# Optimization experiments

Hardware: AMD Instinct MI355X
Metric: run time of the kernel (lower is better)

Reference implementation:

```python
import jax, jax.numpy as jnp
import numpy as np

B, N, H = 4, 4096, 64
T1 = 3072  # num_types = [0, 3072, 1024]


def _xavier(key, shape):
    fan_in, fan_out = shape[1], shape[0]
    lim = float(np.sqrt(6.0 / (fan_in + fan_out)))
    return jax.random.uniform(key, shape, jnp.float32, -lim, lim)


def setup_inputs() -> dict:
    key = jax.random.key(0)
    ks = jax.random.split(key, 16)
    adjacency = (jax.random.uniform(ks[0], (N, N)) < 0.05).astype(jnp.float32)
    adjacency = jnp.maximum(adjacency, jnp.eye(N, dtype=jnp.float32))  # avoid all-zero rows
    return {
        "hidden_states": jax.random.normal(ks[1], (B, N, H), jnp.float32),
        "input_states": jax.random.normal(ks[2], (B, 1, 1), jnp.float32),
        "adjacency": adjacency,
        "Wq": _xavier(ks[3], (H, H)),
        "Wk": _xavier(ks[4], (H, H)),
        "Wv": _xavier(ks[5], (H, H)),
        "Wu_inter": _xavier(ks[6], (H, H)),
        "bu_inter": jnp.zeros((H,), jnp.float32),
        "Wt_inter": _xavier(ks[7], (H, H)),
        "bt_inter": jnp.zeros((H,), jnp.float32),
        "Wu_out": _xavier(ks[8], (H, H)),
        "bu_out": jnp.zeros((H,), jnp.float32),
        "Wt_out": _xavier(ks[9], (H, H)),
        "bt_out": jnp.zeros((H,), jnp.float32),
        "step_size": jnp.float32(0.01),
    }


def reference(hidden_states, input_states, adjacency, Wq, Wk, Wv,
              Wu_inter, bu_inter, Wt_inter, bt_inter,
              Wu_out, bu_out, Wt_out, bt_out, step_size):
    # AccumulatorFunction: adjacency-masked QK^T, L2-norm rows (NOT softmax), aggregate V
    mask = adjacency.T  # [N, N]
    q = hidden_states @ Wq.T  # [B, N, H]
    k = hidden_states @ Wk.T
    v = hidden_states @ Wv.T
    rel = jnp.einsum('bnd,bmd->bnm', q, k) * mask  # [B, N, N]
    rel = rel / jnp.linalg.norm(rel, axis=2, keepdims=True)
    acc = jnp.einsum('bnm,bmd->bnd', rel, v)  # [B, N, H]

    # update_hidden_states with num_types = [0, T1, N - T1]
    def branch(h, a, Wu, bu, Wt, bt):
        dt = 2.0 * jax.nn.sigmoid(h @ Wt.T + bt) - 1.0
        return h + step_size * dt * (a @ Wu.T + bu)

    upd_inter = branch(hidden_states[:, :T1], acc[:, :T1],
                       Wu_inter, bu_inter, Wt_inter, bt_inter)
    upd_out = branch(hidden_states[:, T1:], acc[:, T1:],
                     Wu_out, bu_out, Wt_out, bt_out)
    return jnp.concatenate([upd_inter, upd_out], axis=1)  # [B, N, H]
```

## Files before the change

### kernel.cpp

```cpp
#include <hip/hip_runtime.h>
#include <hip/hip_bf16.h>
#include <math.h>

#define Bb 4
#define Nn 4096
#define Hh 64
#define T1c 3072
#define MC 8

typedef unsigned short ushort_t;
typedef __bf16 bf16x8 __attribute__((ext_vector_type(8)));
typedef float floatx4 __attribute__((ext_vector_type(4)));
typedef float floatx16 __attribute__((ext_vector_type(16)));

__device__ ushort_t g_qw[(size_t)Bb * Nn * Hh];
__device__ ushort_t g_kp[(size_t)Bb * Nn * Hh];
__device__ ushort_t g_vp[(size_t)Bb * Nn * Hh];
__device__ ushort_t g_dt[(size_t)Bb * Nn * Hh];
__device__ unsigned g_bm32[(size_t)(Nn / 32) * Nn];
__device__ ushort_t g_pacH[(size_t)Bb * 64 * MC * 64 * 64];
__device__ float    g_pss[(size_t)Bb * 64 * MC * 64];

__device__ __forceinline__ float bf2f(unsigned short u) {
    union { unsigned int i; float f; } c;
    c.i = ((unsigned int)u) << 16;
    return c.f;
}
__device__ __forceinline__ unsigned short f2bf(float f) {
    union { float f; unsigned int i; } c;
    c.f = f;
    unsigned int x = c.i;
    unsigned int r = (x + 0x7fffu + ((x >> 16) & 1u)) >> 16;
    return (unsigned short)r;
}

__device__ __forceinline__ bf16x8 ld8(const void* p, size_t eidx, bool f32) {
    if (f32) {
        const float* fp = (const float*)p + eidx;
        float4 x0 = *(const float4*)fp;
        float4 x1 = *(const float4*)(fp + 4);
        bf16x8 r;
        r[0] = (__bf16)x0.x; r[1] = (__bf16)x0.y; r[2] = (__bf16)x0.z; r[3] = (__bf16)x0.w;
        r[4] = (__bf16)x1.x; r[5] = (__bf16)x1.y; r[6] = (__bf16)x1.z; r[7] = (__bf16)x1.w;
        return r;
    }
    return *(const bf16x8*)((const ushort_t*)p + eidx);
}
__device__ __forceinline__ float ldS(const void* p, size_t eidx, bool f32) {
    return f32 ? ((const float*)p)[eidx] : bf2f(((const ushort_t*)p)[eidx]);
}
__device__ __forceinline__ void stOut(void* p, size_t eidx, float v, bool f32) {
    if (f32) ((float*)p)[eidx] = v;
    else ((ushort_t*)p)[eidx] = f2bf(v);
}

__device__ __forceinline__ floatx4 mfma16(bf16x8 a, bf16x8 b, floatx4 c) {
    return __builtin_amdgcn_mfma_f32_16x16x32_bf16(a, b, c, 0, 0, 0);
}
__device__ __forceinline__ floatx16 mfma32(bf16x8 a, bf16x8 b, floatx16 c) {
    return __builtin_amdgcn_mfma_f32_32x32x16_bf16(a, b, c, 0, 0, 0);
}

__device__ __forceinline__ float fast_tanh(float x) {
    float e = __expf(-2.0f * fabsf(x));
    float t = (1.0f - e) / (1.0f + e);
    return copysignf(t, x);
}

__global__ __launch_bounds__(256) void prep_kernel(
    const void* __restrict__ hid, const void* __restrict__ adj,
    const void* __restrict__ Wq, const void* __restrict__ Wk,
    const void* __restrict__ Wv,
    const void* __restrict__ Wti, const void* __restrict__ bti,
    const void* __restrict__ Wto, const void* __restrict__ bto)
{
    const bool F32 = (*(const unsigned*)adj) == 0x3F800000u;

    __shared__ __align__(16) ushort_t stage[2][1024];

    if (blockIdx.x >= 1024) {
        const int bi = blockIdx.x - 1024;
        const int mt = bi & 63;
        const int nc = bi >> 6;
        const int n = nc * 256 + threadIdx.x;
        const int m0 = mt * 64;

        unsigned long long bits = 0ull;
#pragma unroll 8
        for (int j = 0; j < 64; ++j) {
            const float v = ldS(adj, (size_t)(m0 + j) * Nn + n, F32);
            bits |= (unsigned long long)(v != 0.f) << j;
        }
        g_bm32[(size_t)(2 * mt) * Nn + n] = (unsigned)(bits & 0xffffffffull);
        g_bm32[(size_t)(2 * mt + 1) * Nn + n] = (unsigned)(bits >> 32);
        return;
    }

    const int bi = blockIdx.x;
    const int b = bi >> 8;
    const int n16 = (bi & 255) << 4;
    const int t = threadIdx.x;
    const int wv = t >> 6, lane = t & 63, l16 = lane & 15, quad = lane >> 4;
    const bool inter = (n16 < T1c);

    const void* W = (wv == 0) ? Wq : (wv == 1) ? Wk : (wv == 2) ? Wv
                    : (inter ? Wti : Wto);
    const void* bt = inter ? bti : bto;

    const size_t hbase = ((size_t)(b * Nn + n16 + l16)) * Hh + quad * 8;
    bf16x8 a0 = ld8(hid, hbase, F32);
    bf16x8 a1 = ld8(hid, hbase + 32, F32);
    floatx4 z = {0.f, 0.f, 0.f, 0.f};

    floatx4 c[4];
#pragma unroll
    for (int ti = 0; ti < 4; ++ti) {
        const size_t wrow = (size_t)(ti * 16 + l16) * 64 + quad * 8;
        bf16x8 w0 = ld8(W, wrow, F32);
        bf16x8 w1 = ld8(W, wrow + 32, F32);
        c[ti] = mfma16(a1, w1, mfma16(a0, w0, z));
    }

    if (wv == 0) {
#pragma unroll
        for (int ti = 0; ti < 4; ++ti)
#pragma unroll
            for (int r = 0; r < 4; ++r)
                g_qw[((size_t)(b * Nn + n16 + quad * 4 + r)) * 64 + ti * 16 + l16] = f2bf(c[ti][r]);
    } else if (wv == 1) {
        ushort_t* st = stage[0];
#pragma unroll
        for (int ti = 0; ti < 4; ++ti)
#pragma unroll
            for (int r = 0; r < 4; ++r)
                st[((ti * 2 + (l16 >> 3)) * 16 + quad * 4 + r) * 8 + (l16 & 7)] = f2bf(c[ti][r]);
        const int mlo0 = n16 & 16;
        const size_t gbase = (size_t)(b * 128 + (n16 >> 5)) * 2048;
#pragma unroll
        for (int piece = 0; piece < 2; ++piece) {
            const int off = lane * 8 + piece * 512;
            const int i = off >> 8;
            const int hh = (off >> 7) & 1;
            const int mj = off & 127;
            *(uint4*)&g_kp[gbase + (size_t)i * 512 + hh * 256 + mlo0 * 8 + mj] =
                *(const uint4*)&st[off];
        }
    } else if (wv == 2) {
        ushort_t* st = stage[1];
#pragma unroll
        for (int ti = 0; ti < 4; ++ti)
#pragma unroll
            for (int r = 0; r < 4; ++r)
                st[(((ti >> 1) * 2 + (quad & 1)) * 32 + (ti & 1) * 16 + l16) * 8
                   + r + 4 * (quad >> 1)] = f2bf(c[ti][r]);
        const size_t gbase = (size_t)(b * 256 + (n16 >> 4)) * 1024;
#pragma unroll
        for (int piece = 0; piece < 2; ++piece) {
            const int off = lane * 8 + piece * 512;
            *(uint4*)&g_vp[gbase + off] = *(const uint4*)&st[off];
        }
    } else {
#pragma unroll
        for (int ti = 0; ti < 4; ++ti) {
            const float btv = ldS(bt, ti * 16 + l16, F32);
#pragma unroll
            for (int r = 0; r < 4; ++r)
                g_dt[((size_t)(b * Nn + n16 + quad * 4 + r)) * 64 + ti * 16 + l16] =
                    f2bf(fast_tanh(0.5f * (c[ti][r] + btv)));
        }
    }
}

__global__ __launch_bounds__(256, 4) void attn_part_kernel()
{
    const int bi = blockIdx.x;
    const int b  = bi >> 8;
    const int mc = (bi >> 5) & 7;
    const int jq = bi & 31;
    const int wv = threadIdx.x >> 6, lane = threadIdx.x & 63;
    const int l32 = lane & 31, h = lane >> 5;
    const int j = jq * 4 + wv;
    const int n0w = j * 32;

    bf16x8 qf[4];
#pragma unroll
    for (int i = 0; i < 4; ++i)
        qf[i] = *(const bf16x8*)&g_qw[((size_t)(b * Nn + n0w + l32)) * 64 + h * 8 + 16 * i];

    floatx16 acc[2];
#pragma unroll
    for (int dt = 0; dt < 2; ++dt)
#pragma unroll
        for (int r = 0; r < 16; ++r) acc[dt][r] = 0.f;
    float ssql = 0.f;

    for (int it = 0; it < 16; ++it) {
        const int mb32 = mc * 16 + it;

        floatx16 s;
#pragma unroll
        for (int r = 0; r < 16; ++r) s[r] = 0.f;
#pragma unroll
        for (int i = 0; i < 4; ++i) {
            bf16x8 kf = *(const bf16x8*)&g_kp[
                ((((size_t)(b * 128 + mb32) * 4 + i) * 2 + h) * 32 + l32) * 8];
            s = mfma32(kf, qf[i], s);
        }

        const unsigned mw = g_bm32[(size_t)mb32 * Nn + n0w + l32];
        bf16x8 af0, af1;
#pragma unroll
        for (int r = 0; r < 16; ++r) {
            const int rp = (r & 3) + 8 * (r >> 2) + 4 * h;
            const float sm = ((mw >> rp) & 1u) ? s[r] : 0.f;
            ssql += sm * sm;
            if (r < 8) af0[r] = (__bf16)sm; else af1[r - 8] = (__bf16)sm;
        }

#pragma unroll
        for (int mb = 0; mb < 2; ++mb) {
            const size_t vb = (((size_t)(b * 256 + mb32 * 2 + mb) * 2) * 2 + h) * 32 * 8;
            bf16x8 vf0 = *(const bf16x8*)&g_vp[vb + (size_t)l32 * 8];
            bf16x8 vf1 = *(const bf16x8*)&g_vp[vb + (2 * 32 * 8) + (size_t)l32 * 8];
            if (mb == 0) {
                acc[0] = mfma32(af0, vf0, acc[0]);
                acc[1] = mfma32(af0, vf1, acc[1]);
            } else {
                acc[0] = mfma32(af1, vf0, acc[0]);
                acc[1] = mfma32(af1, vf1, acc[1]);
            }
        }
    }

    ssql += __shfl_xor(ssql, 32, 64);

    const int nt = n0w >> 6;
    const int nl0 = (j & 1) * 32;
    const size_t pbase = ((size_t)(b * 64 + nt) * MC + mc);
#pragma unroll
    for (int dt = 0; dt < 2; ++dt)
#pragma unroll
        for (int r = 0; r < 16; ++r) {
            const int rp = (r & 3) + 8 * (r >> 2) + 4 * h;
            g_pacH[(pbase * 64 + nl0 + rp) * 64 + dt * 32 + l32] = f2bf(acc[dt][r]);
        }
    if (h == 0) g_pss[pbase * 64 + nl0 + l32] = ssql;
}

__global__ __launch_bounds__(256) void finish_kernel(
    const void* __restrict__ hid, const void* __restrict__ adj,
    const void* __restrict__ Wui, const void* __restrict__ bui,
    const void* __restrict__ Wuo, const void* __restrict__ buo,
    const void* __restrict__ stepp, void* __restrict__ outp)
{
    const bool F32 = (*(const unsigned*)adj) == 0x3F800000u;

    const int bi = blockIdx.x;
    const int b = bi >> 8;
    const int r16 = bi & 255;
    const int n16 = r16 << 4;
    const int nt = r16 >> 2;
    const int nloc0 = (r16 & 3) << 4;
    const int t = threadIdx.x;
    const int wv = t >> 6, lane = t & 63, l16 = lane & 15, quad = lane >> 4;

    float sv = g_pss[((size_t)(b * 64 + nt) * MC + quad) * 64 + nloc0 + l16]
             + g_pss[((size_t)(b * 64 + nt) * MC + quad + 4) * 64 + nloc0 + l16];
    sv += __shfl_xor(sv, 16, 64);
    sv += __shfl_xor(sv, 32, 64);
    const float inv = (sv > 0.f) ? __frsqrt_rn(sv) : 0.f;

    float s0[8], s1[8];
#pragma unroll
    for (int jj = 0; jj < 8; ++jj) { s0[jj] = 0.f; s1[jj] = 0.f; }
#pragma unroll
    for (int mcq = 0; mcq < MC; ++mcq) {
        const size_t abase =
            (((size_t)(b * 64 + nt) * MC + mcq) * 64 + nloc0 + l16) * 64 + quad * 8;
        bf16x8 x = *(const bf16x8*)&g_pacH[abase];
        bf16x8 y = *(const bf16x8*)&g_pacH[abase + 32];
#pragma unroll
        for (int jj = 0; jj < 8; ++jj) {
            s0[jj] += (float)x[jj];
            s1[jj] += (float)y[jj];
        }
    }
    bf16x8 ua0, ua1;
#pragma unroll
    for (int jj = 0; jj < 8; ++jj) {
        ua0[jj] = (__bf16)(s0[jj] * inv);
        ua1[jj] = (__bf16)(s1[jj] * inv);
    }

    const bool inter = (n16 < T1c);
    const void* Wu = inter ? Wui : Wuo;
    const void* bu = inter ? bui : buo;
    const float step = ldS(stepp, 0, F32);

    const int ti = wv;
    floatx4 z = {0.f, 0.f, 0.f, 0.f};
    const size_t wrow = (size_t)(ti * 16 + l16) * 64 + quad * 8;
    bf16x8 w0 = ld8(Wu, wrow, F32);
    bf16x8 w1 = ld8(Wu, wrow + 32, F32);
    floatx4 u = mfma16(ua1, w1, mfma16(ua0, w0, z));
    const float buv = ldS(bu, ti * 16 + l16, F32);
#pragma unroll
    for (int r = 0; r < 4; ++r) {
        const size_t idx = ((size_t)(b * Nn + n16 + quad * 4 + r)) * 64 + ti * 16 + l16;
        const float hv = ldS(hid, idx, F32);
        const float dtv = bf2f(g_dt[idx]);
        stOut(outp, idx, hv + step * dtv * (u[r] + buv), F32);
    }
}

extern "C" void kernel_launch(void* const* d_in, const int* in_sizes, int n_in,
                              void* d_out, int out_size, void* d_ws, size_t ws_size,
                              hipStream_t stream)
{
    const void* hid = d_in[0];
    const void* adj = d_in[2];
    const void* Wq  = d_in[3];
    const void* Wk  = d_in[4];
    const void* Wv  = d_in[5];
    const void* Wui = d_in[6];
    const void* bui = d_in[7];
    const void* Wti = d_in[8];
    const void* bti = d_in[9];
    const void* Wuo = d_in[10];
    const void* buo = d_in[11];
    const void* Wto = d_in[12];
    const void* bto = d_in[13];
    const void* stepp = d_in[14];

    prep_kernel<<<dim3(2048), dim3(256), 0, stream>>>(
        hid, adj, Wq, Wk, Wv, Wti, bti, Wto, bto);
    attn_part_kernel<<<dim3(1024), dim3(256), 0, stream>>>();
    finish_kernel<<<dim3(Bb * (Nn / 16)), dim3(256), 0, stream>>>(
        hid, adj, Wui, bui, Wuo, buo, stepp, d_out);
}
```

Measured before the change: 169.1 us.

## Switch attention partial kernel from 32x32 to 16x16 MFMA tiles with new K/V layouts

The attention partial kernel now gives each wave 16 query rows and uses 16x16x32 MFMAs instead of 32x32x16, doubling the grid to 2048 blocks. The K and V packing in the prep kernel is rewritten to match the new fragment layout, and V is now written directly from registers without LDS staging. The block index order is also changed so that batch varies fastest. The aim is more parallel waves and more occupancy, but each K/V fragment is now reused across fewer query rows, which increases global/L2 traffic per MFMA.

```diff
diff --git a/kernel.cpp b/kernel.cpp
--- a/kernel.cpp
+++ b/kernel.cpp
@@ -11,7 +11,6 @@
 typedef unsigned short ushort_t;
 typedef __bf16 bf16x8 __attribute__((ext_vector_type(8)));
 typedef float floatx4 __attribute__((ext_vector_type(4)));
-typedef float floatx16 __attribute__((ext_vector_type(16)));
 
 __device__ ushort_t g_qw[(size_t)Bb * Nn * Hh];
 __device__ ushort_t g_kp[(size_t)Bb * Nn * Hh];
@@ -57,9 +56,6 @@
 __device__ __forceinline__ floatx4 mfma16(bf16x8 a, bf16x8 b, floatx4 c) {
     return __builtin_amdgcn_mfma_f32_16x16x32_bf16(a, b, c, 0, 0, 0);
 }
-__device__ __forceinline__ floatx16 mfma32(bf16x8 a, bf16x8 b, floatx16 c) {
-    return __builtin_amdgcn_mfma_f32_32x32x16_bf16(a, b, c, 0, 0, 0);
-}
 
 __device__ __forceinline__ float fast_tanh(float x) {
     float e = __expf(-2.0f * fabsf(x));
@@ -76,7 +72,7 @@
 {
     const bool F32 = (*(const unsigned*)adj) == 0x3F800000u;
 
-    __shared__ __align__(16) ushort_t stage[2][1024];
+    __shared__ __align__(16) ushort_t stage[1024];
 
     if (blockIdx.x >= 1024) {
         const int bi = blockIdx.x - 1024;
@@ -128,36 +124,28 @@
             for (int r = 0; r < 4; ++r)
                 g_qw[((size_t)(b * Nn + n16 + quad * 4 + r)) * 64 + ti * 16 + l16] = f2bf(c[ti][r]);
     } else if (wv == 1) {
-        ushort_t* st = stage[0];
 #pragma unroll
         for (int ti = 0; ti < 4; ++ti)
 #pragma unroll
             for (int r = 0; r < 4; ++r)
-                st[((ti * 2 + (l16 >> 3)) * 16 + quad * 4 + r) * 8 + (l16 & 7)] = f2bf(c[ti][r]);
-        const int mlo0 = n16 & 16;
-        const size_t gbase = (size_t)(b * 128 + (n16 >> 5)) * 2048;
+                stage[(ti >> 1) * 512
+                      + (((ti & 1) * 2 + (l16 >> 3)) * 16 + quad * 4 + r) * 8
+                      + (l16 & 7)] = f2bf(c[ti][r]);
+        const size_t gbase = (size_t)(b * 256 + (n16 >> 4)) * 1024;
 #pragma unroll
         for (int piece = 0; piece < 2; ++piece) {
             const int off = lane * 8 + piece * 512;
-            const int i = off >> 8;
-            const int hh = (off >> 7) & 1;
-            const int mj = off & 127;
-            *(uint4*)&g_kp[gbase + (size_t)i * 512 + hh * 256 + mlo0 * 8 + mj] =
-                *(const uint4*)&st[off];
+            *(uint4*)&g_kp[gbase + off] = *(const uint4*)&stage[off];
         }
     } else if (wv == 2) {
-        ushort_t* st = stage[1];
-#pragma unroll
-        for (int ti = 0; ti < 4; ++ti)
-#pragma unroll
-            for (int r = 0; r < 4; ++r)
-                st[(((ti >> 1) * 2 + (quad & 1)) * 32 + (ti & 1) * 16 + l16) * 8
-                   + r + 4 * (quad >> 1)] = f2bf(c[ti][r]);
-        const size_t gbase = (size_t)(b * 256 + (n16 >> 4)) * 1024;
-#pragma unroll
-        for (int piece = 0; piece < 2; ++piece) {
-            const int off = lane * 8 + piece * 512;
-            *(uint4*)&g_vp[gbase + off] = *(const uint4*)&st[off];
+        const int jh = (n16 >> 4) & 1;
+#pragma unroll
+        for (int ti = 0; ti < 4; ++ti) {
+            uint2 pk;
+            pk.x = (unsigned)f2bf(c[ti][0]) | ((unsigned)f2bf(c[ti][1]) << 16);
+            pk.y = (unsigned)f2bf(c[ti][2]) | ((unsigned)f2bf(c[ti][3]) << 16);
+            *(uint2*)&g_vp[((((size_t)(b * 128 + (n16 >> 5)) * 4 + ti) * 64
+                             + quad * 16 + l16) * 8) + 4 * jh] = pk;
         }
     } else {
 #pragma unroll
@@ -171,80 +159,70 @@
     }
 }
 
-__global__ __launch_bounds__(256, 4) void attn_part_kernel()
+__global__ __launch_bounds__(256) void attn_part_kernel()
 {
     const int bi = blockIdx.x;
-    const int b  = bi >> 8;
-    const int mc = (bi >> 5) & 7;
-    const int jq = bi & 31;
+    const int j16q = bi >> 5;
+    const int mc = (bi >> 2) & 7;
+    const int b = bi & 3;
     const int wv = threadIdx.x >> 6, lane = threadIdx.x & 63;
-    const int l32 = lane & 31, h = lane >> 5;
-    const int j = jq * 4 + wv;
-    const int n0w = j * 32;
-
-    bf16x8 qf[4];
-#pragma unroll
-    for (int i = 0; i < 4; ++i)
-        qf[i] = *(const bf16x8*)&g_qw[((size_t)(b * Nn + n0w + l32)) * 64 + h * 8 + 16 * i];
-
-    floatx16 acc[2];
-#pragma unroll
-    for (int dt = 0; dt < 2; ++dt)
-#pragma unroll
-        for (int r = 0; r < 16; ++r) acc[dt][r] = 0.f;
+    const int l16 = lane & 15, quad = lane >> 4;
+    const int j16 = j16q * 4 + wv;
+    const int n0w = j16 * 16;
+
+    bf16x8 qf[2];
+#pragma unroll
+    for (int kc = 0; kc < 2; ++kc)
+        qf[kc] = *(const bf16x8*)&g_qw[((size_t)(b * Nn + n0w + l16)) * 64 + kc * 32 + quad * 8];
+
+    floatx4 z = {0.f, 0.f, 0.f, 0.f};
+    floatx4 acc[4];
+#pragma unroll
+    for (int ti = 0; ti < 4; ++ti) acc[ti] = z;
     float ssql = 0.f;
 
+#pragma unroll 2
     for (int it = 0; it < 16; ++it) {
         const int mb32 = mc * 16 + it;
 
-        floatx16 s;
-#pragma unroll
-        for (int r = 0; r < 16; ++r) s[r] = 0.f;
-#pragma unroll
-        for (int i = 0; i < 4; ++i) {
-            bf16x8 kf = *(const bf16x8*)&g_kp[
-                ((((size_t)(b * 128 + mb32) * 4 + i) * 2 + h) * 32 + l32) * 8];
-            s = mfma32(kf, qf[i], s);
-        }
-
-        const unsigned mw = g_bm32[(size_t)mb32 * Nn + n0w + l32];
-        bf16x8 af0, af1;
-#pragma unroll
-        for (int r = 0; r < 16; ++r) {
-            const int rp = (r & 3) + 8 * (r >> 2) + 4 * h;
-            const float sm = ((mw >> rp) & 1u) ? s[r] : 0.f;
-            ssql += sm * sm;
-            if (r < 8) af0[r] = (__bf16)sm; else af1[r - 8] = (__bf16)sm;
-        }
-
-#pragma unroll
-        for (int mb = 0; mb < 2; ++mb) {
-            const size_t vb = (((size_t)(b * 256 + mb32 * 2 + mb) * 2) * 2 + h) * 32 * 8;
-            bf16x8 vf0 = *(const bf16x8*)&g_vp[vb + (size_t)l32 * 8];
-            bf16x8 vf1 = *(const bf16x8*)&g_vp[vb + (2 * 32 * 8) + (size_t)l32 * 8];
-            if (mb == 0) {
-                acc[0] = mfma32(af0, vf0, acc[0]);
-                acc[1] = mfma32(af0, vf1, acc[1]);
-            } else {
-                acc[0] = mfma32(af1, vf0, acc[0]);
-                acc[1] = mfma32(af1, vf1, acc[1]);
-            }
-        }
-    }
-
+        const size_t kb = (size_t)(b * 256 + 2 * mb32) * 1024 + (size_t)lane * 8;
+        floatx4 slo = z, shi = z;
+        slo = mfma16(*(const bf16x8*)&g_kp[kb], qf[0], slo);
+        slo = mfma16(*(const bf16x8*)&g_kp[kb + 512], qf[1], slo);
+        shi = mfma16(*(const bf16x8*)&g_kp[kb + 1024], qf[0], shi);
+        shi = mfma16(*(const bf16x8*)&g_kp[kb + 1536], qf[1], shi);
+
+        const unsigned mw = g_bm32[(size_t)mb32 * Nn + n0w + l16];
+        bf16x8 af;
+#pragma unroll
+        for (int r = 0; r < 4; ++r) {
+            const int rp = quad * 4 + r;
+            const float smlo = ((mw >> rp) & 1u) ? slo[r] : 0.f;
+            const float smhi = ((mw >> (rp + 16)) & 1u) ? shi[r] : 0.f;
+            ssql += smlo * smlo + smhi * smhi;
+            af[r] = (__bf16)smlo;
+            af[r + 4] = (__bf16)smhi;
+        }
+
+        const size_t vb = (size_t)(b * 128 + mb32) * 2048 + (size_t)lane * 8;
+#pragma unroll
+        for (int ti = 0; ti < 4; ++ti)
+            acc[ti] = mfma16(af, *(const bf16x8*)&g_vp[vb + (size_t)ti * 512], acc[ti]);
+    }
+
+    ssql += __shfl_xor(ssql, 16, 64);
     ssql += __shfl_xor(ssql, 32, 64);
 
-    const int nt = n0w >> 6;
-    const int nl0 = (j & 1) * 32;
+    const int nt = j16 >> 2;
+    const int nl0 = (j16 & 3) * 16;
     const size_t pbase = ((size_t)(b * 64 + nt) * MC + mc);
-#pragma unroll
-    for (int dt = 0; dt < 2; ++dt)
-#pragma unroll
-        for (int r = 0; r < 16; ++r) {
-            const int rp = (r & 3) + 8 * (r >> 2) + 4 * h;
-            g_pacH[(pbase * 64 + nl0 + rp) * 64 + dt * 32 + l32] = f2bf(acc[dt][r]);
-        }
-    if (h == 0) g_pss[pbase * 64 + nl0 + l32] = ssql;
+    if (lane < 16) g_pss[pbase * 64 + nl0 + lane] = ssql;
+
+#pragma unroll
+    for (int ti = 0; ti < 4; ++ti)
+#pragma unroll
+        for (int r = 0; r < 4; ++r)
+            g_pacH[(pbase * 64 + nl0 + quad * 4 + r) * 64 + ti * 16 + l16] = f2bf(acc[ti][r]);
 }
 
 __global__ __launch_bounds__(256) void finish_kernel(
@@ -334,7 +312,7 @@
 
     prep_kernel<<<dim3(2048), dim3(256), 0, stream>>>(
         hid, adj, Wq, Wk, Wv, Wti, bti, Wto, bto);
-    attn_part_kernel<<<dim3(1024), dim3(256), 0, stream>>>();
+    attn_part_kernel<<<dim3(2048), dim3(256), 0, stream>>>();
     finish_kernel<<<dim3(Bb * (Nn / 16)), dim3(256), 0, stream>>>(
         hid, adj, Wui, bui, Wuo, buo, stepp, d_out);
 }
```

New measurement: 183.6 us. +8.6%, slower.
